# Kernel optimization log

Hardware: AMD Instinct MI355X
Metric: run time of the kernel (lower is better)

## Reference

```python
import jax, jax.numpy as jnp
import numpy as np

B, S, V, E, H = 128, 128, 8000, 512, 2048
GIVEN = 64


def setup_inputs() -> dict:
    key = jax.random.key(0)
    ks = jax.random.split(key, 13)
    def p(i, shape):
        return (jax.random.normal(ks[i], shape, jnp.float32) * 0.02)
    return {
        "x": jax.random.randint(ks[0], (B, S), 0, V, jnp.int32),
        "class_label": jax.random.randint(ks[1], (B,), 0, 2, jnp.int32),
        "given_num": GIVEN,
        "emb": p(2, (V, E)),
        "Wih0": p(3, (4 * H, E)), "Whh0": p(4, (4 * H, H)),
        "bih0": p(5, (4 * H,)), "bhh0": p(6, (4 * H,)),
        "Wih1": p(7, (4 * H, H)), "Whh1": p(8, (4 * H, H)),
        "bih1": p(9, (4 * H,)), "bhh1": p(10, (4 * H,)),
        "Wlin": p(11, (V, H)), "blin": p(12, (V,)),
    }


def _cell(xt, h, c, Wih, Whh, bih, bhh):
    # PyTorch LSTMCell math, gate order (i, f, g, o)
    g = xt @ Wih.T + h @ Whh.T + (bih + bhh)
    i, f, gg, o = jnp.split(g, 4, axis=-1)
    c = jax.nn.sigmoid(f) * c + jax.nn.sigmoid(i) * jnp.tanh(gg)
    h = jax.nn.sigmoid(o) * jnp.tanh(c)
    return h, c


def reference(x, class_label, given_num, emb, Wih0, Whh0, bih0, bhh0,
              Wih1, Whh1, bih1, bhh1, Wlin, blin):
    Bb, Ss = x.shape
    Hh = Whh0.shape[1]
    z = jnp.zeros((Bb, Hh), dtype=emb.dtype)
    init = (z, z, z, z)  # (h0, c0, h1, c1) for 2-layer LSTM

    def two_layer(carry, te):
        h0, c0, h1, c1 = carry
        h0, c0 = _cell(te, h0, c0, Wih0, Whh0, bih0, bhh0)
        h1, c1 = _cell(h0, h1, c1, Wih1, Whh1, bih1, bhh1)
        return (h0, c0, h1, c1)

    # Teacher-forced prefix: feed ground-truth tokens for i < given_num
    seq_e = emb[x[:, :given_num]]  # (B, given_num, E)
    def tf_step(carry, te):
        return two_layer(carry, te), None
    carry, _ = jax.lax.scan(tf_step, init, seq_e.swapaxes(0, 1))

    # Rollout: sample from softmax(logits) each step (multinomial == categorical)
    te0 = emb[x[:, given_num - 1]]  # (B, E)
    keys = jax.random.split(jax.random.key(1), Ss - given_num)

    def roll_step(carry, k):
        (h0, c0, h1, c1), te = carry
        h0, c0, h1, c1 = two_layer((h0, c0, h1, c1), te)
        logits = h1 @ Wlin.T + blin  # (B, V)
        nt = jax.random.categorical(k, logits)  # (B,)
        return ((h0, c0, h1, c1), emb[nt]), nt

    _, toks = jax.lax.scan(roll_step, (carry, te0), keys)  # (S-given, B)
    return jnp.concatenate([x[:, :given_num], toks.T.astype(x.dtype)], axis=1)
```

## Files before the change

### kernel.cpp

```cpp
#include <hip/hip_runtime.h>
#include <stdint.h>
#include <math.h>

#define B_     128
#define S_     128
#define V_     8000
#define E_     512
#define H_     2048
#define H4_    8192
#define GIVEN_ 64

typedef __bf16 bf16x8 __attribute__((ext_vector_type(8)));
typedef float  f32x16 __attribute__((ext_vector_type(16)));
typedef short  short8 __attribute__((ext_vector_type(8)));

__device__ __forceinline__ uint32_t rotl32(uint32_t v, int d) {
  return (v << d) | (v >> (32 - d));
}

__device__ __forceinline__ void threefry2x32(uint32_t k0, uint32_t k1,
                                             uint32_t x0, uint32_t x1,
                                             uint32_t& o0, uint32_t& o1) {
  uint32_t k2 = k0 ^ k1 ^ 0x1BD11BDAu;
  x0 += k0; x1 += k1;
#define TF_RND(R) { x0 += x1; x1 = rotl32(x1, (R)); x1 ^= x0; }
  TF_RND(13) TF_RND(15) TF_RND(26) TF_RND(6)
  x0 += k1; x1 += k2 + 1u;
  TF_RND(17) TF_RND(29) TF_RND(16) TF_RND(24)
  x0 += k2; x1 += k0 + 2u;
  TF_RND(13) TF_RND(15) TF_RND(26) TF_RND(6)
  x0 += k0; x1 += k1 + 3u;
  TF_RND(17) TF_RND(29) TF_RND(16) TF_RND(24)
  x0 += k1; x1 += k2 + 4u;
  TF_RND(13) TF_RND(15) TF_RND(26) TF_RND(6)
  x0 += k2; x1 += k0 + 5u;
#undef TF_RND
  o0 = x0; o1 = x1;
}

__global__ void keys_kernel(uint32_t* __restrict__ keys) {
  int t = threadIdx.x;
  uint32_t o0, o1;
  threefry2x32(0u, 1u, 0u, (uint32_t)t, o0, o1);
  keys[2 * t]     = o0;
  keys[2 * t + 1] = o1;
}

__global__ void copy_prefix(const int* __restrict__ x, int* __restrict__ out) {
  int idx = blockIdx.x * blockDim.x + threadIdx.x;
  int b = idx >> 6;
  int s = idx & 63;
  out[b * S_ + s] = x[b * S_ + s];
}

__device__ __forceinline__ void split2(float x, uint16_t& hi, uint16_t& lo) {
  uint32_t xb = __float_as_uint(x);
  hi = (uint16_t)(xb >> 16);
  float l = x - __uint_as_float(xb & 0xFFFF0000u);
  lo = (uint16_t)(__float_as_uint(l) >> 16);
}

__device__ __forceinline__ void splitpack(float4 a, float4 b,
                                          bf16x8& hi, bf16x8& lo) {
  float e[8] = {a.x, a.y, a.z, a.w, b.x, b.y, b.z, b.w};
  short8 h, l;
#pragma unroll
  for (int j = 0; j < 8; ++j) {
    uint16_t h16, l16;
    split2(e[j], h16, l16);
    h[j] = (short)h16;
    l[j] = (short)l16;
  }
  hi = __builtin_bit_cast(bf16x8, h);
  lo = __builtin_bit_cast(bf16x8, l);
}

__device__ __forceinline__ void unpack3(short8 hv, uint2 m, bf16x8& bh, bf16x8& bl) {
  short8 lv;
#pragma unroll
  for (int j = 0; j < 8; ++j) {
    uint32_t hbits = ((uint32_t)(uint16_t)hv[j]) << 16;
    uint32_t mbyte = ((j < 4 ? (m.x >> (8 * j)) : (m.y >> (8 * (j - 4)))) & 0xFFu);
    float xf = __uint_as_float(hbits | (mbyte << 8));
    float lf = xf - __uint_as_float(hbits);
    lv[j] = (short)(__float_as_uint(lf) >> 16);
  }
  bh = __builtin_bit_cast(bf16x8, hv);
  bl = __builtin_bit_cast(bf16x8, lv);
}

__global__ __launch_bounds__(256) void pack3(
    const float* __restrict__ W, uint16_t* __restrict__ PH,
    uint8_t* __restrict__ PM, int n8)
{
  int i = blockIdx.x * 256 + threadIdx.x;
  if (i >= n8) return;
  float4 a = ((const float4*)W)[2 * i];
  float4 b = ((const float4*)W)[2 * i + 1];
  float e[8] = {a.x, a.y, a.z, a.w, b.x, b.y, b.z, b.w};
  short8 h;
  uint32_t mlo = 0, mhi = 0;
#pragma unroll
  for (int j = 0; j < 8; ++j) {
    uint32_t xb = __float_as_uint(e[j]);
    h[j] = (short)(xb >> 16);
    uint32_t mb = (xb >> 8) & 0xFFu;
    if (j < 4) mlo |= mb << (8 * j);
    else       mhi |= mb << (8 * (j - 4));
  }
  *(short8*)&PH[(size_t)i * 8] = h;
  *(uint2*)&PM[(size_t)i * 8] = make_uint2(mlo, mhi);
}

#define MFMA_(a, b, c) __builtin_amdgcn_mfma_f32_32x32x16_bf16(a, b, c, 0, 0, 0)

template<bool GATHER>
__device__ __forceinline__ void run_phase_p(
    f32x16 (&acc)[4],
    const float* __restrict__ aF,
    const uint16_t* __restrict__ aHi, const uint16_t* __restrict__ aLo,
    const int* __restrict__ ridx, int rstride,
    const uint16_t* __restrict__ PH, const uint8_t* __restrict__ PM,
    int K, bool gateRe, int jb, int w, int lrow, int lgrp)
{
  const int nFS = K >> 7;
  const int wrow = gateRe ? ((lrow >> 3) * H_ + jb * 8 + (lrow & 7))
                          : (jb * 32 + lrow);
  const size_t bbase = (size_t)wrow * K + lgrp * 8;

  size_t aoff0, aoff1, aoff2, aoff3;
  if (GATHER) {
    aoff0 = (size_t)ridx[(size_t)(lrow)      * rstride] * E_ + lgrp * 8;
    aoff1 = (size_t)ridx[(size_t)(32 + lrow) * rstride] * E_ + lgrp * 8;
    aoff2 = (size_t)ridx[(size_t)(64 + lrow) * rstride] * E_ + lgrp * 8;
    aoff3 = (size_t)ridx[(size_t)(96 + lrow) * rstride] * E_ + lgrp * 8;
  } else {
    aoff0 = (size_t)lgrp * 256 + (size_t)lrow * 8;
    aoff1 = aoff0 + 512;
    aoff2 = aoff0 + 1024;
    aoff3 = aoff0 + 1536;
  }

  short8 bH[2]; uint2 bM[2];
  float4 gR0[2][2], gR1[2][2], gR2[2][2], gR3[2][2];
  bf16x8 sh0[2], sh1[2], sh2[2], sh3[2], sl0[2], sl1[2], sl2[2], sl3[2];

#define LOADFS(BUF, KS)                                                      \
  {                                                                          \
    const size_t bo = bbase + (size_t)(KS) * 16;                             \
    bH[BUF] = *(const short8*)(PH + bo);                                     \
    bM[BUF] = *(const uint2*)(PM + bo);                                      \
    if (GATHER) {                                                            \
      const float* a0 = aF + aoff0 + (size_t)(KS) * 16;                      \
      const float* a1 = aF + aoff1 + (size_t)(KS) * 16;                      \
      const float* a2 = aF + aoff2 + (size_t)(KS) * 16;                      \
      const float* a3 = aF + aoff3 + (size_t)(KS) * 16;                      \
      gR0[BUF][0] = ((const float4*)a0)[0]; gR0[BUF][1] = ((const float4*)a0)[1]; \
      gR1[BUF][0] = ((const float4*)a1)[0]; gR1[BUF][1] = ((const float4*)a1)[1]; \
      gR2[BUF][0] = ((const float4*)a2)[0]; gR2[BUF][1] = ((const float4*)a2)[1]; \
      gR3[BUF][0] = ((const float4*)a3)[0]; gR3[BUF][1] = ((const float4*)a3)[1]; \
    } else {                                                                 \
      size_t o0 = aoff0 + (size_t)(KS) * 2048;                               \
      size_t o1 = aoff1 + (size_t)(KS) * 2048;                               \
      size_t o2 = aoff2 + (size_t)(KS) * 2048;                               \
      size_t o3 = aoff3 + (size_t)(KS) * 2048;                               \
      sh0[BUF] = *(const bf16x8*)(aHi + o0); sl0[BUF] = *(const bf16x8*)(aLo + o0); \
      sh1[BUF] = *(const bf16x8*)(aHi + o1); sl1[BUF] = *(const bf16x8*)(aLo + o1); \
      sh2[BUF] = *(const bf16x8*)(aHi + o2); sl2[BUF] = *(const bf16x8*)(aLo + o2); \
      sh3[BUF] = *(const bf16x8*)(aHi + o3); sl3[BUF] = *(const bf16x8*)(aLo + o3); \
    }                                                                        \
  }

#define COMPFS(BUF)                                                          \
  {                                                                          \
    bf16x8 bh, bl;                                                           \
    unpack3(bH[BUF], bM[BUF], bh, bl);                                       \
    bf16x8 ah, al;                                                           \
    if (GATHER) splitpack(gR0[BUF][0], gR0[BUF][1], ah, al);                 \
    else { ah = sh0[BUF]; al = sl0[BUF]; }                                   \
    acc[0] = MFMA_(ah, bh, acc[0]);                                          \
    acc[0] = MFMA_(ah, bl, acc[0]);                                          \
    acc[0] = MFMA_(al, bh, acc[0]);                                          \
    if (GATHER) splitpack(gR1[BUF][0], gR1[BUF][1], ah, al);                 \
    else { ah = sh1[BUF]; al = sl1[BUF]; }                                   \
    acc[1] = MFMA_(ah, bh, acc[1]);                                          \
    acc[1] = MFMA_(ah, bl, acc[1]);                                          \
    acc[1] = MFMA_(al, bh, acc[1]);                                          \
    if (GATHER) splitpack(gR2[BUF][0], gR2[BUF][1], ah, al);                 \
    else { ah = sh2[BUF]; al = sl2[BUF]; }                                   \
    acc[2] = MFMA_(ah, bh, acc[2]);                                          \
    acc[2] = MFMA_(ah, bl, acc[2]);                                          \
    acc[2] = MFMA_(al, bh, acc[2]);                                          \
    if (GATHER) splitpack(gR3[BUF][0], gR3[BUF][1], ah, al);                 \
    else { ah = sh3[BUF]; al = sl3[BUF]; }                                   \
    acc[3] = MFMA_(ah, bh, acc[3]);                                          \
    acc[3] = MFMA_(ah, bl, acc[3]);                                          \
    acc[3] = MFMA_(al, bh, acc[3]);                                          \
  }

  int ks = w;
  LOADFS(0, ks); ks += 8;
  int rem = nFS;
  while (rem >= 2) {
    LOADFS(1, ks); ks += 8;
    COMPFS(0);
    if (rem > 2) { LOADFS(0, ks); ks += 8; }
    COMPFS(1);
    rem -= 2;
  }
#undef LOADFS
#undef COMPFS
}

template<int EPI, int GATHER1>
__global__ __launch_bounds__(512, 2) void gemm_ks_p(
    const float* __restrict__ a1F,
    const uint16_t* __restrict__ a1Hi, const uint16_t* __restrict__ a1Lo,
    const int* __restrict__ ridx, int rstride,
    const uint16_t* __restrict__ PH1, const uint8_t* __restrict__ PM1, int K1,
    const uint16_t* __restrict__ a2Hi, const uint16_t* __restrict__ a2Lo,
    const uint16_t* __restrict__ PH2, const uint8_t* __restrict__ PM2, int K2,
    const float* __restrict__ bih, const float* __restrict__ bhh,
    float* __restrict__ cState,
    uint16_t* __restrict__ hOutHi, uint16_t* __restrict__ hOutLo,
    const float* __restrict__ bias, float* __restrict__ Cout)
{
  __shared__ float red[4][128 * 32];

  const int jb   = blockIdx.x;
  const int tid  = threadIdx.x;
  const int w    = tid >> 6;
  const int lane = tid & 63;
  const int lrow = lane & 31;
  const int lgrp = lane >> 5;

  f32x16 acc[4];
#pragma unroll
  for (int mf = 0; mf < 4; ++mf)
#pragma unroll
    for (int r = 0; r < 16; ++r) acc[mf][r] = 0.0f;

  run_phase_p<GATHER1 != 0>(acc, a1F, a1Hi, a1Lo, ridx, rstride,
                            PH1, PM1, K1, EPI == 1, jb, w, lrow, lgrp);
  if (K2 > 0)
    run_phase_p<false>(acc, nullptr, a2Hi, a2Lo, nullptr, 0,
                       PH2, PM2, K2, EPI == 1, jb, w, lrow, lgrp);

  const int wl = w & 3;
  if (w < 4) {
#pragma unroll
    for (int mf = 0; mf < 4; ++mf)
#pragma unroll
      for (int r = 0; r < 16; ++r) {
        const int row = mf * 32 + (r & 3) + 8 * (r >> 2) + 4 * lgrp;
        red[wl][row * 32 + (lrow ^ (row & 31))] = acc[mf][r];
      }
  }
  __syncthreads();
  if (w >= 4) {
#pragma unroll
    for (int mf = 0; mf < 4; ++mf)
#pragma unroll
      for (int r = 0; r < 16; ++r) {
        const int row = mf * 32 + (r & 3) + 8 * (r >> 2) + 4 * lgrp;
        red[wl][row * 32 + (lrow ^ (row & 31))] += acc[mf][r];
      }
  }
  __syncthreads();

  if constexpr (EPI == 1) {
    const int b  = tid & 127;
    const int uh = (tid >> 7) * 2;
#pragma unroll
    for (int q = 0; q < 2; ++q) {
      const int u = uh + q;
      float gs[4];
#pragma unroll
      for (int g = 0; g < 4; ++g) {
        const int cs = (g * 8 + u) ^ (b & 31);
        gs[g] = ((red[0][b * 32 + cs] + red[1][b * 32 + cs])
                 + red[2][b * 32 + cs]) + red[3][b * 32 + cs];
      }
      const int n = jb * 8 + u;
      float gi = gs[0] + bih[n]          + bhh[n];
      float gf = gs[1] + bih[H_ + n]     + bhh[H_ + n];
      float gg = gs[2] + bih[2 * H_ + n] + bhh[2 * H_ + n];
      float go = gs[3] + bih[3 * H_ + n] + bhh[3 * H_ + n];
      float si = 1.f / (1.f + expf(-gi));
      float sf = 1.f / (1.f + expf(-gf));
      float so = 1.f / (1.f + expf(-go));
      const size_t ci = (size_t)b * H_ + n;
      float cv = sf * cState[ci] + si * tanhf(gg);
      cState[ci] = cv;
      float hv = so * tanhf(cv);
      uint16_t hh, hl;
      split2(hv, hh, hl);
      const size_t hoff = (size_t)((n >> 4) * 4 + (b >> 5)) * 512
                        + (size_t)((n >> 3) & 1) * 256
                        + (size_t)(b & 31) * 8 + (size_t)(n & 7);
      hOutHi[hoff] = hh;
      hOutLo[hoff] = hl;
    }
  } else {
    const int b  = tid & 127;
    const int ch = (tid >> 7) * 8;
#pragma unroll
    for (int q = 0; q < 8; ++q) {
      const int col = ch + q;
      const int cs  = col ^ (b & 31);
      float v = ((red[0][b * 32 + cs] + red[1][b * 32 + cs])
                 + red[2][b * 32 + cs]) + red[3][b * 32 + cs];
      Cout[(size_t)b * V_ + jb * 32 + col] = v + bias[jb * 32 + col];
    }
  }
}

template<bool GATHER>
__device__ __forceinline__ void run_phase_f(
    f32x16 (&acc)[4],
    const float* __restrict__ aF,
    const uint16_t* __restrict__ aHi, const uint16_t* __restrict__ aLo,
    const int* __restrict__ ridx, int rstride,
    const float* __restrict__ W, int K, bool gateRe,
    int jb, int w, int lrow, int lgrp)
{
  const int nFS = K >> 7;
  const int wrow = gateRe ? ((lrow >> 3) * H_ + jb * 8 + (lrow & 7))
                          : (jb * 32 + lrow);
  const float* bptr = W + (size_t)wrow * K + lgrp * 8;

  size_t aoff0, aoff1, aoff2, aoff3;
  if (GATHER) {
    aoff0 = (size_t)ridx[(size_t)(lrow)      * rstride] * E_ + lgrp * 8;
    aoff1 = (size_t)ridx[(size_t)(32 + lrow) * rstride] * E_ + lgrp * 8;
    aoff2 = (size_t)ridx[(size_t)(64 + lrow) * rstride] * E_ + lgrp * 8;
    aoff3 = (size_t)ridx[(size_t)(96 + lrow) * rstride] * E_ + lgrp * 8;
  } else {
    aoff0 = (size_t)lgrp * 256 + (size_t)lrow * 8;
    aoff1 = aoff0 + 512;
    aoff2 = aoff0 + 1024;
    aoff3 = aoff0 + 1536;
  }

  float4 bR0[2], bR1[2];
  float4 gR0[2][2], gR1[2][2], gR2[2][2], gR3[2][2];
  bf16x8 sh0[2], sh1[2], sh2[2], sh3[2], sl0[2], sl1[2], sl2[2], sl3[2];

#define LOADFS(BUF, KS)                                                      \
  {                                                                          \
    const float* bp = bptr + (size_t)(KS) * 16;                              \
    bR0[BUF] = ((const float4*)bp)[0];                                       \
    bR1[BUF] = ((const float4*)bp)[1];                                       \
    if (GATHER) {                                                            \
      const float* a0 = aF + aoff0 + (size_t)(KS) * 16;                      \
      const float* a1 = aF + aoff1 + (size_t)(KS) * 16;                      \
      const float* a2 = aF + aoff2 + (size_t)(KS) * 16;                      \
      const float* a3 = aF + aoff3 + (size_t)(KS) * 16;                      \
      gR0[BUF][0] = ((const float4*)a0)[0]; gR0[BUF][1] = ((const float4*)a0)[1]; \
      gR1[BUF][0] = ((const float4*)a1)[0]; gR1[BUF][1] = ((const float4*)a1)[1]; \
      gR2[BUF][0] = ((const float4*)a2)[0]; gR2[BUF][1] = ((const float4*)a2)[1]; \
      gR3[BUF][0] = ((const float4*)a3)[0]; gR3[BUF][1] = ((const float4*)a3)[1]; \
    } else {                                                                 \
      size_t o0 = aoff0 + (size_t)(KS) * 2048;                               \
      size_t o1 = aoff1 + (size_t)(KS) * 2048;                               \
      size_t o2 = aoff2 + (size_t)(KS) * 2048;                               \
      size_t o3 = aoff3 + (size_t)(KS) * 2048;                               \
      sh0[BUF] = *(const bf16x8*)(aHi + o0); sl0[BUF] = *(const bf16x8*)(aLo + o0); \
      sh1[BUF] = *(const bf16x8*)(aHi + o1); sl1[BUF] = *(const bf16x8*)(aLo + o1); \
      sh2[BUF] = *(const bf16x8*)(aHi + o2); sl2[BUF] = *(const bf16x8*)(aLo + o2); \
      sh3[BUF] = *(const bf16x8*)(aHi + o3); sl3[BUF] = *(const bf16x8*)(aLo + o3); \
    }                                                                        \
  }

#define COMPFS(BUF)                                                          \
  {                                                                          \
    bf16x8 bh, bl;                                                           \
    splitpack(bR0[BUF], bR1[BUF], bh, bl);                                   \
    bf16x8 ah, al;                                                           \
    if (GATHER) splitpack(gR0[BUF][0], gR0[BUF][1], ah, al);                 \
    else { ah = sh0[BUF]; al = sl0[BUF]; }                                   \
    acc[0] = MFMA_(ah, bh, acc[0]);                                          \
    acc[0] = MFMA_(ah, bl, acc[0]);                                          \
    acc[0] = MFMA_(al, bh, acc[0]);                                          \
    if (GATHER) splitpack(gR1[BUF][0], gR1[BUF][1], ah, al);                 \
    else { ah = sh1[BUF]; al = sl1[BUF]; }                                   \
    acc[1] = MFMA_(ah, bh, acc[1]);                                          \
    acc[1] = MFMA_(ah, bl, acc[1]);                                          \
    acc[1] = MFMA_(al, bh, acc[1]);                                          \
    if (GATHER) splitpack(gR2[BUF][0], gR2[BUF][1], ah, al);                 \
    else { ah = sh2[BUF]; al = sl2[BUF]; }                                   \
    acc[2] = MFMA_(ah, bh, acc[2]);                                          \
    acc[2] = MFMA_(ah, bl, acc[2]);                                          \
    acc[2] = MFMA_(al, bh, acc[2]);                                          \
    if (GATHER) splitpack(gR3[BUF][0], gR3[BUF][1], ah, al);                 \
    else { ah = sh3[BUF]; al = sl3[BUF]; }                                   \
    acc[3] = MFMA_(ah, bh, acc[3]);                                          \
    acc[3] = MFMA_(ah, bl, acc[3]);                                          \
    acc[3] = MFMA_(al, bh, acc[3]);                                          \
  }

  int ks = w;
  LOADFS(0, ks); ks += 8;
  int rem = nFS;
  while (rem >= 2) {
    LOADFS(1, ks); ks += 8;
    COMPFS(0);
    if (rem > 2) { LOADFS(0, ks); ks += 8; }
    COMPFS(1);
    rem -= 2;
  }
#undef LOADFS
#undef COMPFS
}

template<int EPI, int GATHER1>
__global__ __launch_bounds__(512, 2) void gemm_ks_f(
    const float* __restrict__ a1F,
    const uint16_t* __restrict__ a1Hi, const uint16_t* __restrict__ a1Lo,
    const int* __restrict__ ridx, int rstride,
    const float* __restrict__ W1, int K1,
    const uint16_t* __restrict__ a2Hi, const uint16_t* __restrict__ a2Lo,
    const float* __restrict__ W2, int K2,
    const float* __restrict__ bih, const float* __restrict__ bhh,
    float* __restrict__ cState,
    uint16_t* __restrict__ hOutHi, uint16_t* __restrict__ hOutLo,
    const float* __restrict__ bias, float* __restrict__ Cout)
{
  __shared__ float red[4][128 * 32];

  const int jb   = blockIdx.x;
  const int tid  = threadIdx.x;
  const int w    = tid >> 6;
  const int lane = tid & 63;
  const int lrow = lane & 31;
  const int lgrp = lane >> 5;

  f32x16 acc[4];
#pragma unroll
  for (int mf = 0; mf < 4; ++mf)
#pragma unroll
    for (int r = 0; r < 16; ++r) acc[mf][r] = 0.0f;

  run_phase_f<GATHER1 != 0>(acc, a1F, a1Hi, a1Lo, ridx, rstride,
                            W1, K1, EPI == 1, jb, w, lrow, lgrp);
  if (K2 > 0)
    run_phase_f<false>(acc, nullptr, a2Hi, a2Lo, nullptr, 0,
                       W2, K2, EPI == 1, jb, w, lrow, lgrp);

  const int wl = w & 3;
  if (w < 4) {
#pragma unroll
    for (int mf = 0; mf < 4; ++mf)
#pragma unroll
      for (int r = 0; r < 16; ++r) {
        const int row = mf * 32 + (r & 3) + 8 * (r >> 2) + 4 * lgrp;
        red[wl][row * 32 + (lrow ^ (row & 31))] = acc[mf][r];
      }
  }
  __syncthreads();
  if (w >= 4) {
#pragma unroll
    for (int mf = 0; mf < 4; ++mf)
#pragma unroll
      for (int r = 0; r < 16; ++r) {
        const int row = mf * 32 + (r & 3) + 8 * (r >> 2) + 4 * lgrp;
        red[wl][row * 32 + (lrow ^ (row & 31))] += acc[mf][r];
      }
  }
  __syncthreads();

  if constexpr (EPI == 1) {
    const int b  = tid & 127;
    const int uh = (tid >> 7) * 2;
#pragma unroll
    for (int q = 0; q < 2; ++q) {
      const int u = uh + q;
      float gs[4];
#pragma unroll
      for (int g = 0; g < 4; ++g) {
        const int cs = (g * 8 + u) ^ (b & 31);
        gs[g] = ((red[0][b * 32 + cs] + red[1][b * 32 + cs])
                 + red[2][b * 32 + cs]) + red[3][b * 32 + cs];
      }
      const int n = jb * 8 + u;
      float gi = gs[0] + bih[n]          + bhh[n];
      float gf = gs[1] + bih[H_ + n]     + bhh[H_ + n];
      float gg = gs[2] + bih[2 * H_ + n] + bhh[2 * H_ + n];
      float go = gs[3] + bih[3 * H_ + n] + bhh[3 * H_ + n];
      float si = 1.f / (1.f + expf(-gi));
      float sf = 1.f / (1.f + expf(-gf));
      float so = 1.f / (1.f + expf(-go));
      const size_t ci = (size_t)b * H_ + n;
      float cv = sf * cState[ci] + si * tanhf(gg);
      cState[ci] = cv;
      float hv = so * tanhf(cv);
      uint16_t hh, hl;
      split2(hv, hh, hl);
      const size_t hoff = (size_t)((n >> 4) * 4 + (b >> 5)) * 512
                        + (size_t)((n >> 3) & 1) * 256
                        + (size_t)(b & 31) * 8 + (size_t)(n & 7);
      hOutHi[hoff] = hh;
      hOutLo[hoff] = hl;
    }
  } else {
    const int b  = tid & 127;
    const int ch = (tid >> 7) * 8;
#pragma unroll
    for (int q = 0; q < 8; ++q) {
      const int col = ch + q;
      const int cs  = col ^ (b & 31);
      float v = ((red[0][b * 32 + cs] + red[1][b * 32 + cs])
                 + red[2][b * 32 + cs]) + red[3][b * 32 + cs];
      Cout[(size_t)b * V_ + jb * 32 + col] = v + bias[jb * 32 + col];
    }
  }
}

__global__ __launch_bounds__(256) void sample_kernel(
    const float* __restrict__ logits, const uint32_t* __restrict__ keys,
    int t, int* __restrict__ out, int col)
{
  const int b = blockIdx.x;
  const int tid = threadIdx.x;
  const uint32_t k0 = keys[2 * t];
  const uint32_t k1 = keys[2 * t + 1];
  const float* lrow = logits + (size_t)b * V_;

  float best = -3.4e38f;
  int bestIdx = 0;
  for (int v = tid; v < V_; v += 256) {
    uint32_t j = (uint32_t)(b * V_ + v);
    uint32_t o0, o1;
    threefry2x32(k0, k1, 0u, j, o0, o1);
    uint32_t bits = o0 ^ o1;
    float f = __uint_as_float((bits >> 9) | 0x3f800000u) - 1.0f;
    float u = fmaxf(1.17549435e-38f, f + 1.17549435e-38f);
    float t1 = (float)log((double)u);
    float t2 = -t1;
    float t3 = (float)log((double)t2);
    float val = (-t3) + lrow[v];
    if (val > best) { best = val; bestIdx = v; }
  }

  __shared__ float sv[256];
  __shared__ int   si[256];
  sv[tid] = best; si[tid] = bestIdx;
  __syncthreads();
  for (int s = 128; s > 0; s >>= 1) {
    if (tid < s) {
      float v2 = sv[tid + s]; int i2 = si[tid + s];
      if (v2 > sv[tid] || (v2 == sv[tid] && i2 < si[tid])) { sv[tid] = v2; si[tid] = i2; }
    }
    __syncthreads();
  }
  if (tid == 0) out[b * S_ + col] = si[0];
}

extern "C" void kernel_launch(void* const* d_in, const int* in_sizes, int n_in,
                              void* d_out, int out_size, void* d_ws, size_t ws_size,
                              hipStream_t stream) {
  const int*   x    = (const int*)  d_in[0];
  const float* emb  = (const float*)d_in[3];
  const float* Wih0 = (const float*)d_in[4];
  const float* Whh0 = (const float*)d_in[5];
  const float* bih0 = (const float*)d_in[6];
  const float* bhh0 = (const float*)d_in[7];
  const float* Wih1 = (const float*)d_in[8];
  const float* Whh1 = (const float*)d_in[9];
  const float* bih1 = (const float*)d_in[10];
  const float* bhh1 = (const float*)d_in[11];
  const float* Wlin = (const float*)d_in[12];
  const float* blin = (const float*)d_in[13];
  int* out = (int*)d_out;

  char* wp = (char*)d_ws;
  size_t o = 0;
  auto alloc = [&](size_t bytes) {
    void* p = wp + o; o += (bytes + 255) & ~(size_t)255; return p;
  };
  uint32_t* keys   = (uint32_t*)alloc(512);
  float*    logits = (float*)   alloc((size_t)B_ * V_ * 4);
  float*    c0     = (float*)   alloc((size_t)B_ * H_ * 4);
  float*    c1     = (float*)   alloc((size_t)B_ * H_ * 4);
  uint16_t* hS0hi[2]; uint16_t* hS0lo[2]; uint16_t* hS1hi[2]; uint16_t* hS1lo[2];
  for (int i = 0; i < 2; ++i) hS0hi[i] = (uint16_t*)alloc((size_t)B_ * H_ * 2);
  for (int i = 0; i < 2; ++i) hS0lo[i] = (uint16_t*)alloc((size_t)B_ * H_ * 2);
  for (int i = 0; i < 2; ++i) hS1hi[i] = (uint16_t*)alloc((size_t)B_ * H_ * 2);
  for (int i = 0; i < 2; ++i) hS1lo[i] = (uint16_t*)alloc((size_t)B_ * H_ * 2);
  size_t zeroBytes = (size_t)((char*)hS1lo[1] + (size_t)B_ * H_ * 2 - (char*)c0);

  const size_t nIh0 = (size_t)H4_ * E_;
  const size_t nHh  = (size_t)H4_ * H_;
  const size_t nLin = (size_t)V_ * H_;
  uint16_t* PHih0 = (uint16_t*)alloc(nIh0 * 2);
  uint8_t*  PMih0 = (uint8_t*) alloc(nIh0);
  uint16_t* PHhh0 = (uint16_t*)alloc(nHh * 2);
  uint8_t*  PMhh0 = (uint8_t*) alloc(nHh);
  uint16_t* PHih1 = (uint16_t*)alloc(nHh * 2);
  uint8_t*  PMih1 = (uint8_t*) alloc(nHh);
  uint16_t* PHhh1 = (uint16_t*)alloc(nHh * 2);
  uint8_t*  PMhh1 = (uint8_t*) alloc(nHh);
  uint16_t* PHlin = (uint16_t*)alloc(nLin * 2);
  uint8_t*  PMlin = (uint8_t*) alloc(nLin);
  const bool usePacked = (o <= ws_size);

  hipMemsetAsync(c0, 0, zeroBytes, stream);
  keys_kernel<<<1, 64, 0, stream>>>(keys);
  copy_prefix<<<(B_ * GIVEN_) / 256, 256, 0, stream>>>(x, out);

  if (usePacked) {
    pack3<<<(int)((nIh0 / 8 + 255) / 256), 256, 0, stream>>>(Wih0, PHih0, PMih0, (int)(nIh0 / 8));
    pack3<<<(int)((nHh / 8 + 255) / 256), 256, 0, stream>>>(Whh0, PHhh0, PMhh0, (int)(nHh / 8));
    pack3<<<(int)((nHh / 8 + 255) / 256), 256, 0, stream>>>(Wih1, PHih1, PMih1, (int)(nHh / 8));
    pack3<<<(int)((nHh / 8 + 255) / 256), 256, 0, stream>>>(Whh1, PHhh1, PMhh1, (int)(nHh / 8));
    pack3<<<(int)((nLin / 8 + 255) / 256), 256, 0, stream>>>(Wlin, PHlin, PMlin, (int)(nLin / 8));
  }

  int p = 0;
  auto lstm_step = [&](const int* ridx) {
    if (usePacked) {
      gemm_ks_p<1, 1><<<H_ / 8, 512, 0, stream>>>(
          emb, nullptr, nullptr, ridx, S_, PHih0, PMih0, E_,
          hS0hi[p], hS0lo[p], PHhh0, PMhh0, H_,
          bih0, bhh0, c0, hS0hi[p ^ 1], hS0lo[p ^ 1], nullptr, nullptr);
      gemm_ks_p<1, 0><<<H_ / 8, 512, 0, stream>>>(
          nullptr, hS0hi[p ^ 1], hS0lo[p ^ 1], nullptr, 0, PHih1, PMih1, H_,
          hS1hi[p], hS1lo[p], PHhh1, PMhh1, H_,
          bih1, bhh1, c1, hS1hi[p ^ 1], hS1lo[p ^ 1], nullptr, nullptr);
    } else {
      gemm_ks_f<1, 1><<<H_ / 8, 512, 0, stream>>>(
          emb, nullptr, nullptr, ridx, S_, Wih0, E_,
          hS0hi[p], hS0lo[p], Whh0, H_,
          bih0, bhh0, c0, hS0hi[p ^ 1], hS0lo[p ^ 1], nullptr, nullptr);
      gemm_ks_f<1, 0><<<H_ / 8, 512, 0, stream>>>(
          nullptr, hS0hi[p ^ 1], hS0lo[p ^ 1], nullptr, 0, Wih1, H_,
          hS1hi[p], hS1lo[p], Whh1, H_,
          bih1, bhh1, c1, hS1hi[p ^ 1], hS1lo[p ^ 1], nullptr, nullptr);
    }
    p ^= 1;
  };

  for (int t = 0; t < GIVEN_; ++t) {
    lstm_step(x + t);
  }

  for (int t = 0; t < S_ - GIVEN_; ++t) {
    const int* ridx = (t == 0) ? (x + (GIVEN_ - 1)) : (out + (GIVEN_ + t - 1));
    lstm_step(ridx);
    if (usePacked) {
      gemm_ks_p<0, 0><<<V_ / 32, 512, 0, stream>>>(
          nullptr, hS1hi[p], hS1lo[p], nullptr, 0, PHlin, PMlin, H_,
          nullptr, nullptr, nullptr, nullptr, 0,
          nullptr, nullptr, nullptr, nullptr, nullptr, blin, logits);
    } else {
      gemm_ks_f<0, 0><<<V_ / 32, 512, 0, stream>>>(
          nullptr, hS1hi[p], hS1lo[p], nullptr, 0, Wlin, H_,
          nullptr, nullptr, nullptr, 0,
          nullptr, nullptr, nullptr, nullptr, nullptr, blin, logits);
    }
    sample_kernel<<<B_, 256, 0, stream>>>(logits, keys, t, out, GIVEN_ + t);
  }
}
```

Before: 12.72 ms.

## Retile packed GEMM to 64x64 output tiles with 2D grid and deeper prefetch

The packed-weight GEMM kernel moves from a 128-batch by 32-column tile to a 64x64 tile, with a second grid dimension splitting the batch into two halves. Each wave now runs a 2x2 set of MFMA accumulators, so every loaded weight fragment is reused across two batch fragments and every activation fragment across two weight fragments. Weight loads are prefetched four k-steps ahead instead of one. The block count stays the same for the LSTM gates and drops from 250 to 250 (125x2) for the logits, but each block reads half the batch and twice the weight rows, which doubles total weight traffic across blocks while cutting per-block activation reuse pressure. The change also raises register use and depends on the new gate interleave and hidden-state store layout being correct.

```diff
diff --git a/kernel.cpp b/kernel.cpp
--- a/kernel.cpp
+++ b/kernel.cpp
@@ -115,18 +115,244 @@
 #define MFMA_(a, b, c) __builtin_amdgcn_mfma_f32_32x32x16_bf16(a, b, c, 0, 0, 0)
 
 template<bool GATHER>
-__device__ __forceinline__ void run_phase_p(
+__device__ __forceinline__ void run_phase64_p(
+    f32x16 (&acc)[2][2],
+    const float* __restrict__ aF,
+    const uint16_t* __restrict__ aHi, const uint16_t* __restrict__ aLo,
+    int tok0, int tok1,
+    const uint16_t* __restrict__ PH, const uint8_t* __restrict__ PM,
+    int K, bool gateRe, int jb, int mb, int w, int lrow, int lgrp)
+{
+  const int nFS = K >> 7;
+  const int c0 = lrow, c1 = 32 + lrow;
+  const int wrow0 = gateRe ? ((c0 >> 4) * H_ + jb * 16 + (c0 & 15)) : (jb * 64 + c0);
+  const int wrow1 = gateRe ? ((c1 >> 4) * H_ + jb * 16 + (c1 & 15)) : (jb * 64 + c1);
+  const size_t bb0 = (size_t)wrow0 * K + lgrp * 8;
+  const size_t bb1 = (size_t)wrow1 * K + lgrp * 8;
+
+  size_t aoff0, aoff1;
+  if (GATHER) {
+    aoff0 = (size_t)tok0 * E_ + lgrp * 8;
+    aoff1 = (size_t)tok1 * E_ + lgrp * 8;
+  } else {
+    aoff0 = (size_t)(mb * 2) * 512 + (size_t)lgrp * 256 + (size_t)lrow * 8;
+    aoff1 = aoff0 + 512;
+  }
+
+  short8 bH0[4], bH1[4]; uint2 bM0[4], bM1[4];
+  float4 gA0[2][2], gA1[2][2];
+  bf16x8 sh0[2], sh1[2], sl0[2], sl1[2];
+
+#define BLOAD(BUF, KS)                                                       \
+  {                                                                          \
+    const size_t o0 = bb0 + (size_t)(KS) * 16;                               \
+    const size_t o1 = bb1 + (size_t)(KS) * 16;                               \
+    bH0[BUF] = *(const short8*)(PH + o0);                                    \
+    bM0[BUF] = *(const uint2*)(PM + o0);                                     \
+    bH1[BUF] = *(const short8*)(PH + o1);                                    \
+    bM1[BUF] = *(const uint2*)(PM + o1);                                     \
+  }
+
+#define ALOAD(BUF, KS)                                                       \
+  {                                                                          \
+    if (GATHER) {                                                            \
+      const float* a0 = aF + aoff0 + (size_t)(KS) * 16;                      \
+      const float* a1 = aF + aoff1 + (size_t)(KS) * 16;                      \
+      gA0[BUF][0] = ((const float4*)a0)[0];                                  \
+      gA0[BUF][1] = ((const float4*)a0)[1];                                  \
+      gA1[BUF][0] = ((const float4*)a1)[0];                                  \
+      gA1[BUF][1] = ((const float4*)a1)[1];                                  \
+    } else {                                                                 \
+      size_t o0 = aoff0 + (size_t)(KS) * 2048;                               \
+      size_t o1 = aoff1 + (size_t)(KS) * 2048;                               \
+      sh0[BUF] = *(const bf16x8*)(aHi + o0);                                 \
+      sl0[BUF] = *(const bf16x8*)(aLo + o0);                                 \
+      sh1[BUF] = *(const bf16x8*)(aHi + o1);                                 \
+      sl1[BUF] = *(const bf16x8*)(aLo + o1);                                 \
+    }                                                                        \
+  }
+
+#define COMP(BB, AB)                                                         \
+  {                                                                          \
+    bf16x8 bh0, bl0, bh1, bl1;                                               \
+    unpack3(bH0[BB], bM0[BB], bh0, bl0);                                     \
+    unpack3(bH1[BB], bM1[BB], bh1, bl1);                                     \
+    bf16x8 ah0, al0, ah1, al1;                                               \
+    if (GATHER) {                                                            \
+      splitpack(gA0[AB][0], gA0[AB][1], ah0, al0);                           \
+      splitpack(gA1[AB][0], gA1[AB][1], ah1, al1);                           \
+    } else {                                                                 \
+      ah0 = sh0[AB]; al0 = sl0[AB];                                          \
+      ah1 = sh1[AB]; al1 = sl1[AB];                                          \
+    }                                                                        \
+    acc[0][0] = MFMA_(ah0, bh0, acc[0][0]);                                  \
+    acc[0][0] = MFMA_(ah0, bl0, acc[0][0]);                                  \
+    acc[0][0] = MFMA_(al0, bh0, acc[0][0]);                                  \
+    acc[0][1] = MFMA_(ah0, bh1, acc[0][1]);                                  \
+    acc[0][1] = MFMA_(ah0, bl1, acc[0][1]);                                  \
+    acc[0][1] = MFMA_(al0, bh1, acc[0][1]);                                  \
+    acc[1][0] = MFMA_(ah1, bh0, acc[1][0]);                                  \
+    acc[1][0] = MFMA_(ah1, bl0, acc[1][0]);                                  \
+    acc[1][0] = MFMA_(al1, bh0, acc[1][0]);                                  \
+    acc[1][1] = MFMA_(ah1, bh1, acc[1][1]);                                  \
+    acc[1][1] = MFMA_(ah1, bl1, acc[1][1]);                                  \
+    acc[1][1] = MFMA_(al1, bh1, acc[1][1]);                                  \
+  }
+
+  BLOAD(0, w); BLOAD(1, w + 8); BLOAD(2, w + 16); BLOAD(3, w + 24);
+  ALOAD(0, w); ALOAD(1, w + 8);
+  for (int it = 0; it < nFS; it += 4) {
+    const int kb = w + it * 8;
+    COMP(0, 0);
+    if (it + 4 < nFS) BLOAD(0, kb + 32);
+    if (it + 2 < nFS) ALOAD(0, kb + 16);
+    COMP(1, 1);
+    if (it + 5 < nFS) BLOAD(1, kb + 40);
+    if (it + 3 < nFS) ALOAD(1, kb + 24);
+    COMP(2, 0);
+    if (it + 6 < nFS) BLOAD(2, kb + 48);
+    if (it + 4 < nFS) ALOAD(0, kb + 32);
+    COMP(3, 1);
+    if (it + 7 < nFS) BLOAD(3, kb + 56);
+    if (it + 5 < nFS) ALOAD(1, kb + 40);
+  }
+#undef BLOAD
+#undef ALOAD
+#undef COMP
+}
+
+template<int EPI, int GATHER1>
+__global__ __launch_bounds__(512, 2) void gemm_ks_p(
+    const float* __restrict__ a1F,
+    const uint16_t* __restrict__ a1Hi, const uint16_t* __restrict__ a1Lo,
+    const int* __restrict__ ridx, int rstride,
+    const uint16_t* __restrict__ PH1, const uint8_t* __restrict__ PM1, int K1,
+    const uint16_t* __restrict__ a2Hi, const uint16_t* __restrict__ a2Lo,
+    const uint16_t* __restrict__ PH2, const uint8_t* __restrict__ PM2, int K2,
+    const float* __restrict__ bih, const float* __restrict__ bhh,
+    float* __restrict__ cState,
+    uint16_t* __restrict__ hOutHi, uint16_t* __restrict__ hOutLo,
+    const float* __restrict__ bias, float* __restrict__ Cout)
+{
+  __shared__ float red[4][64 * 64];
+
+  const int jb   = blockIdx.x;
+  const int mb   = blockIdx.y;
+  const int tid  = threadIdx.x;
+  const int w    = tid >> 6;
+  const int lane = tid & 63;
+  const int lrow = lane & 31;
+  const int lgrp = lane >> 5;
+
+  f32x16 acc[2][2];
+#pragma unroll
+  for (int i = 0; i < 2; ++i)
+#pragma unroll
+    for (int j = 0; j < 2; ++j)
+#pragma unroll
+      for (int r = 0; r < 16; ++r) acc[i][j][r] = 0.0f;
+
+  if (GATHER1) {
+    const int tok0 = ridx[(size_t)(mb * 64 + lrow) * rstride];
+    const int tok1 = ridx[(size_t)(mb * 64 + 32 + lrow) * rstride];
+    run_phase64_p<true>(acc, a1F, nullptr, nullptr, tok0, tok1,
+                        PH1, PM1, K1, EPI == 1, jb, mb, w, lrow, lgrp);
+  } else {
+    run_phase64_p<false>(acc, nullptr, a1Hi, a1Lo, 0, 0,
+                         PH1, PM1, K1, EPI == 1, jb, mb, w, lrow, lgrp);
+  }
+  if (K2 > 0)
+    run_phase64_p<false>(acc, nullptr, a2Hi, a2Lo, 0, 0,
+                         PH2, PM2, K2, EPI == 1, jb, mb, w, lrow, lgrp);
+
+  const int wl = w & 3;
+  if (w < 4) {
+#pragma unroll
+    for (int mf = 0; mf < 2; ++mf)
+#pragma unroll
+      for (int nf = 0; nf < 2; ++nf)
+#pragma unroll
+        for (int r = 0; r < 16; ++r) {
+          const int row = mf * 32 + (r & 3) + 8 * (r >> 2) + 4 * lgrp;
+          red[wl][row * 64 + nf * 32 + (lrow ^ (row & 31))] = acc[mf][nf][r];
+        }
+  }
+  __syncthreads();
+  if (w >= 4) {
+#pragma unroll
+    for (int mf = 0; mf < 2; ++mf)
+#pragma unroll
+      for (int nf = 0; nf < 2; ++nf)
+#pragma unroll
+        for (int r = 0; r < 16; ++r) {
+          const int row = mf * 32 + (r & 3) + 8 * (r >> 2) + 4 * lgrp;
+          red[wl][row * 64 + nf * 32 + (lrow ^ (row & 31))] += acc[mf][nf][r];
+        }
+  }
+  __syncthreads();
+
+  if constexpr (EPI == 1) {
+    const int b    = tid & 63;
+    const int brow = mb * 64 + b;
+    const int uh   = tid >> 6;
+#pragma unroll
+    for (int q = 0; q < 2; ++q) {
+      const int u = uh * 2 + q;
+      float gs[4];
+#pragma unroll
+      for (int g = 0; g < 4; ++g) {
+        const int cs = (g * 16 + u) ^ (b & 31);
+        gs[g] = ((red[0][b * 64 + cs] + red[1][b * 64 + cs])
+                 + red[2][b * 64 + cs]) + red[3][b * 64 + cs];
+      }
+      const int n = jb * 16 + u;
+      float gi = gs[0] + bih[n]          + bhh[n];
+      float gf = gs[1] + bih[H_ + n]     + bhh[H_ + n];
+      float gg = gs[2] + bih[2 * H_ + n] + bhh[2 * H_ + n];
+      float go = gs[3] + bih[3 * H_ + n] + bhh[3 * H_ + n];
+      float si = 1.f / (1.f + expf(-gi));
+      float sf = 1.f / (1.f + expf(-gf));
+      float so = 1.f / (1.f + expf(-go));
+      const size_t ci = (size_t)brow * H_ + n;
+      float cv = sf * cState[ci] + si * tanhf(gg);
+      cState[ci] = cv;
+      float hv = so * tanhf(cv);
+      uint16_t hh, hl;
+      split2(hv, hh, hl);
+      const size_t hoff = (size_t)((n >> 4) * 4 + (brow >> 5)) * 512
+                        + (size_t)((n >> 3) & 1) * 256
+                        + (size_t)(brow & 31) * 8 + (size_t)(n & 7);
+      hOutHi[hoff] = hh;
+      hOutLo[hoff] = hl;
+    }
+  } else {
+    const int b  = tid & 63;
+    const int bg = mb * 64 + b;
+    const int ch = (tid >> 6) * 8;
+#pragma unroll
+    for (int q = 0; q < 8; ++q) {
+      const int col = ch + q;
+      const int cs  = col ^ (b & 31);
+      float v = ((red[0][b * 64 + cs] + red[1][b * 64 + cs])
+                 + red[2][b * 64 + cs]) + red[3][b * 64 + cs];
+      Cout[(size_t)bg * V_ + jb * 64 + col] = v + bias[jb * 64 + col];
+    }
+  }
+}
+
+template<bool GATHER>
+__device__ __forceinline__ void run_phase_f(
     f32x16 (&acc)[4],
     const float* __restrict__ aF,
     const uint16_t* __restrict__ aHi, const uint16_t* __restrict__ aLo,
     const int* __restrict__ ridx, int rstride,
-    const uint16_t* __restrict__ PH, const uint8_t* __restrict__ PM,
-    int K, bool gateRe, int jb, int w, int lrow, int lgrp)
+    const float* __restrict__ W, int K, bool gateRe,
+    int jb, int w, int lrow, int lgrp)
 {
   const int nFS = K >> 7;
   const int wrow = gateRe ? ((lrow >> 3) * H_ + jb * 8 + (lrow & 7))
                           : (jb * 32 + lrow);
-  const size_t bbase = (size_t)wrow * K + lgrp * 8;
+  const float* bptr = W + (size_t)wrow * K + lgrp * 8;
 
   size_t aoff0, aoff1, aoff2, aoff3;
   if (GATHER) {
@@ -141,15 +367,15 @@
     aoff3 = aoff0 + 1536;
   }
 
-  short8 bH[2]; uint2 bM[2];
+  float4 bR0[2], bR1[2];
   float4 gR0[2][2], gR1[2][2], gR2[2][2], gR3[2][2];
   bf16x8 sh0[2], sh1[2], sh2[2], sh3[2], sl0[2], sl1[2], sl2[2], sl3[2];
 
 #define LOADFS(BUF, KS)                                                      \
   {                                                                          \
-    const size_t bo = bbase + (size_t)(KS) * 16;                             \
-    bH[BUF] = *(const short8*)(PH + bo);                                     \
-    bM[BUF] = *(const uint2*)(PM + bo);                                      \
+    const float* bp = bptr + (size_t)(KS) * 16;                              \
+    bR0[BUF] = ((const float4*)bp)[0];                                       \
+    bR1[BUF] = ((const float4*)bp)[1];                                       \
     if (GATHER) {                                                            \
       const float* a0 = aF + aoff0 + (size_t)(KS) * 16;                      \
       const float* a1 = aF + aoff1 + (size_t)(KS) * 16;                      \
@@ -174,7 +400,7 @@
 #define COMPFS(BUF)                                                          \
   {                                                                          \
     bf16x8 bh, bl;                                                           \
-    unpack3(bH[BUF], bM[BUF], bh, bl);                                       \
+    splitpack(bR0[BUF], bR1[BUF], bh, bl);                                   \
     bf16x8 ah, al;                                                           \
     if (GATHER) splitpack(gR0[BUF][0], gR0[BUF][1], ah, al);                 \
     else { ah = sh0[BUF]; al = sl0[BUF]; }                                   \
@@ -213,13 +439,13 @@
 }
 
 template<int EPI, int GATHER1>
-__global__ __launch_bounds__(512, 2) void gemm_ks_p(
+__global__ __launch_bounds__(512, 2) void gemm_ks_f(
     const float* __restrict__ a1F,
     const uint16_t* __restrict__ a1Hi, const uint16_t* __restrict__ a1Lo,
     const int* __restrict__ ridx, int rstride,
-    const uint16_t* __restrict__ PH1, const uint8_t* __restrict__ PM1, int K1,
+    const float* __restrict__ W1, int K1,
     const uint16_t* __restrict__ a2Hi, const uint16_t* __restrict__ a2Lo,
-    const uint16_t* __restrict__ PH2, const uint8_t* __restrict__ PM2, int K2,
+    const float* __restrict__ W2, int K2,
     const float* __restrict__ bih, const float* __restrict__ bhh,
     float* __restrict__ cState,
     uint16_t* __restrict__ hOutHi, uint16_t* __restrict__ hOutLo,
@@ -240,11 +466,11 @@
 #pragma unroll
     for (int r = 0; r < 16; ++r) acc[mf][r] = 0.0f;
 
-  run_phase_p<GATHER1 != 0>(acc, a1F, a1Hi, a1Lo, ridx, rstride,
-                            PH1, PM1, K1, EPI == 1, jb, w, lrow, lgrp);
+  run_phase_f<GATHER1 != 0>(acc, a1F, a1Hi, a1Lo, ridx, rstride,
+                            W1, K1, EPI == 1, jb, w, lrow, lgrp);
   if (K2 > 0)
-    run_phase_p<false>(acc, nullptr, a2Hi, a2Lo, nullptr, 0,
-                       PH2, PM2, K2, EPI == 1, jb, w, lrow, lgrp);
+    run_phase_f<false>(acc, nullptr, a2Hi, a2Lo, nullptr, 0,
+                       W2, K2, EPI == 1, jb, w, lrow, lgrp);
 
   const int wl = w & 3;
   if (w < 4) {
@@ -315,207 +541,6 @@
   }
 }
 
-template<bool GATHER>
-__device__ __forceinline__ void run_phase_f(
-    f32x16 (&acc)[4],
-    const float* __restrict__ aF,
-    const uint16_t* __restrict__ aHi, const uint16_t* __restrict__ aLo,
-    const int* __restrict__ ridx, int rstride,
-    const float* __restrict__ W, int K, bool gateRe,
-    int jb, int w, int lrow, int lgrp)
-{
-  const int nFS = K >> 7;
-  const int wrow = gateRe ? ((lrow >> 3) * H_ + jb * 8 + (lrow & 7))
-                          : (jb * 32 + lrow);
-  const float* bptr = W + (size_t)wrow * K + lgrp * 8;
-
-  size_t aoff0, aoff1, aoff2, aoff3;
-  if (GATHER) {
-    aoff0 = (size_t)ridx[(size_t)(lrow)      * rstride] * E_ + lgrp * 8;
-    aoff1 = (size_t)ridx[(size_t)(32 + lrow) * rstride] * E_ + lgrp * 8;
-    aoff2 = (size_t)ridx[(size_t)(64 + lrow) * rstride] * E_ + lgrp * 8;
-    aoff3 = (size_t)ridx[(size_t)(96 + lrow) * rstride] * E_ + lgrp * 8;
-  } else {
-    aoff0 = (size_t)lgrp * 256 + (size_t)lrow * 8;
-    aoff1 = aoff0 + 512;
-    aoff2 = aoff0 + 1024;
-    aoff3 = aoff0 + 1536;
-  }
-
-  float4 bR0[2], bR1[2];
-  float4 gR0[2][2], gR1[2][2], gR2[2][2], gR3[2][2];
-  bf16x8 sh0[2], sh1[2], sh2[2], sh3[2], sl0[2], sl1[2], sl2[2], sl3[2];
-
-#define LOADFS(BUF, KS)                                                      \
-  {                                                                          \
-    const float* bp = bptr + (size_t)(KS) * 16;                              \
-    bR0[BUF] = ((const float4*)bp)[0];                                       \
-    bR1[BUF] = ((const float4*)bp)[1];                                       \
-    if (GATHER) {                                                            \
-      const float* a0 = aF + aoff0 + (size_t)(KS) * 16;                      \
-      const float* a1 = aF + aoff1 + (size_t)(KS) * 16;                      \
-      const float* a2 = aF + aoff2 + (size_t)(KS) * 16;                      \
-      const float* a3 = aF + aoff3 + (size_t)(KS) * 16;                      \
-      gR0[BUF][0] = ((const float4*)a0)[0]; gR0[BUF][1] = ((const float4*)a0)[1]; \
-      gR1[BUF][0] = ((const float4*)a1)[0]; gR1[BUF][1] = ((const float4*)a1)[1]; \
-      gR2[BUF][0] = ((const float4*)a2)[0]; gR2[BUF][1] = ((const float4*)a2)[1]; \
-      gR3[BUF][0] = ((const float4*)a3)[0]; gR3[BUF][1] = ((const float4*)a3)[1]; \
-    } else {                                                                 \
-      size_t o0 = aoff0 + (size_t)(KS) * 2048;                               \
-      size_t o1 = aoff1 + (size_t)(KS) * 2048;                               \
-      size_t o2 = aoff2 + (size_t)(KS) * 2048;                               \
-      size_t o3 = aoff3 + (size_t)(KS) * 2048;                               \
-      sh0[BUF] = *(const bf16x8*)(aHi + o0); sl0[BUF] = *(const bf16x8*)(aLo + o0); \
-      sh1[BUF] = *(const bf16x8*)(aHi + o1); sl1[BUF] = *(const bf16x8*)(aLo + o1); \
-      sh2[BUF] = *(const bf16x8*)(aHi + o2); sl2[BUF] = *(const bf16x8*)(aLo + o2); \
-      sh3[BUF] = *(const bf16x8*)(aHi + o3); sl3[BUF] = *(const bf16x8*)(aLo + o3); \
-    }                                                                        \
-  }
-
-#define COMPFS(BUF)                                                          \
-  {                                                                          \
-    bf16x8 bh, bl;                                                           \
-    splitpack(bR0[BUF], bR1[BUF], bh, bl);                                   \
-    bf16x8 ah, al;                                                           \
-    if (GATHER) splitpack(gR0[BUF][0], gR0[BUF][1], ah, al);                 \
-    else { ah = sh0[BUF]; al = sl0[BUF]; }                                   \
-    acc[0] = MFMA_(ah, bh, acc[0]);                                          \
-    acc[0] = MFMA_(ah, bl, acc[0]);                                          \
-    acc[0] = MFMA_(al, bh, acc[0]);                                          \
-    if (GATHER) splitpack(gR1[BUF][0], gR1[BUF][1], ah, al);                 \
-    else { ah = sh1[BUF]; al = sl1[BUF]; }                                   \
-    acc[1] = MFMA_(ah, bh, acc[1]);                                          \
-    acc[1] = MFMA_(ah, bl, acc[1]);                                          \
-    acc[1] = MFMA_(al, bh, acc[1]);                                          \
-    if (GATHER) splitpack(gR2[BUF][0], gR2[BUF][1], ah, al);                 \
-    else { ah = sh2[BUF]; al = sl2[BUF]; }                                   \
-    acc[2] = MFMA_(ah, bh, acc[2]);                                          \
-    acc[2] = MFMA_(ah, bl, acc[2]);                                          \
-    acc[2] = MFMA_(al, bh, acc[2]);                                          \
-    if (GATHER) splitpack(gR3[BUF][0], gR3[BUF][1], ah, al);                 \
-    else { ah = sh3[BUF]; al = sl3[BUF]; }                                   \
-    acc[3] = MFMA_(ah, bh, acc[3]);                                          \
-    acc[3] = MFMA_(ah, bl, acc[3]);                                          \
-    acc[3] = MFMA_(al, bh, acc[3]);                                          \
-  }
-
-  int ks = w;
-  LOADFS(0, ks); ks += 8;
-  int rem = nFS;
-  while (rem >= 2) {
-    LOADFS(1, ks); ks += 8;
-    COMPFS(0);
-    if (rem > 2) { LOADFS(0, ks); ks += 8; }
-    COMPFS(1);
-    rem -= 2;
-  }
-#undef LOADFS
-#undef COMPFS
-}
-
-template<int EPI, int GATHER1>
-__global__ __launch_bounds__(512, 2) void gemm_ks_f(
-    const float* __restrict__ a1F,
-    const uint16_t* __restrict__ a1Hi, const uint16_t* __restrict__ a1Lo,
-    const int* __restrict__ ridx, int rstride,
-    const float* __restrict__ W1, int K1,
-    const uint16_t* __restrict__ a2Hi, const uint16_t* __restrict__ a2Lo,
-    const float* __restrict__ W2, int K2,
-    const float* __restrict__ bih, const float* __restrict__ bhh,
-    float* __restrict__ cState,
-    uint16_t* __restrict__ hOutHi, uint16_t* __restrict__ hOutLo,
-    const float* __restrict__ bias, float* __restrict__ Cout)
-{
-  __shared__ float red[4][128 * 32];
-
-  const int jb   = blockIdx.x;
-  const int tid  = threadIdx.x;
-  const int w    = tid >> 6;
-  const int lane = tid & 63;
-  const int lrow = lane & 31;
-  const int lgrp = lane >> 5;
-
-  f32x16 acc[4];
-#pragma unroll
-  for (int mf = 0; mf < 4; ++mf)
-#pragma unroll
-    for (int r = 0; r < 16; ++r) acc[mf][r] = 0.0f;
-
-  run_phase_f<GATHER1 != 0>(acc, a1F, a1Hi, a1Lo, ridx, rstride,
-                            W1, K1, EPI == 1, jb, w, lrow, lgrp);
-  if (K2 > 0)
-    run_phase_f<false>(acc, nullptr, a2Hi, a2Lo, nullptr, 0,
-                       W2, K2, EPI == 1, jb, w, lrow, lgrp);
-
-  const int wl = w & 3;
-  if (w < 4) {
-#pragma unroll
-    for (int mf = 0; mf < 4; ++mf)
-#pragma unroll
-      for (int r = 0; r < 16; ++r) {
-        const int row = mf * 32 + (r & 3) + 8 * (r >> 2) + 4 * lgrp;
-        red[wl][row * 32 + (lrow ^ (row & 31))] = acc[mf][r];
-      }
-  }
-  __syncthreads();
-  if (w >= 4) {
-#pragma unroll
-    for (int mf = 0; mf < 4; ++mf)
-#pragma unroll
-      for (int r = 0; r < 16; ++r) {
-        const int row = mf * 32 + (r & 3) + 8 * (r >> 2) + 4 * lgrp;
-        red[wl][row * 32 + (lrow ^ (row & 31))] += acc[mf][r];
-      }
-  }
-  __syncthreads();
-
-  if constexpr (EPI == 1) {
-    const int b  = tid & 127;
-    const int uh = (tid >> 7) * 2;
-#pragma unroll
-    for (int q = 0; q < 2; ++q) {
-      const int u = uh + q;
-      float gs[4];
-#pragma unroll
-      for (int g = 0; g < 4; ++g) {
-        const int cs = (g * 8 + u) ^ (b & 31);
-        gs[g] = ((red[0][b * 32 + cs] + red[1][b * 32 + cs])
-                 + red[2][b * 32 + cs]) + red[3][b * 32 + cs];
-      }
-      const int n = jb * 8 + u;
-      float gi = gs[0] + bih[n]          + bhh[n];
-      float gf = gs[1] + bih[H_ + n]     + bhh[H_ + n];
-      float gg = gs[2] + bih[2 * H_ + n] + bhh[2 * H_ + n];
-      float go = gs[3] + bih[3 * H_ + n] + bhh[3 * H_ + n];
-      float si = 1.f / (1.f + expf(-gi));
-      float sf = 1.f / (1.f + expf(-gf));
-      float so = 1.f / (1.f + expf(-go));
-      const size_t ci = (size_t)b * H_ + n;
-      float cv = sf * cState[ci] + si * tanhf(gg);
-      cState[ci] = cv;
-      float hv = so * tanhf(cv);
-      uint16_t hh, hl;
-      split2(hv, hh, hl);
-      const size_t hoff = (size_t)((n >> 4) * 4 + (b >> 5)) * 512
-                        + (size_t)((n >> 3) & 1) * 256
-                        + (size_t)(b & 31) * 8 + (size_t)(n & 7);
-      hOutHi[hoff] = hh;
-      hOutLo[hoff] = hl;
-    }
-  } else {
-    const int b  = tid & 127;
-    const int ch = (tid >> 7) * 8;
-#pragma unroll
-    for (int q = 0; q < 8; ++q) {
-      const int col = ch + q;
-      const int cs  = col ^ (b & 31);
-      float v = ((red[0][b * 32 + cs] + red[1][b * 32 + cs])
-                 + red[2][b * 32 + cs]) + red[3][b * 32 + cs];
-      Cout[(size_t)b * V_ + jb * 32 + col] = v + bias[jb * 32 + col];
-    }
-  }
-}
-
 __global__ __launch_bounds__(256) void sample_kernel(
     const float* __restrict__ logits, const uint32_t* __restrict__ keys,
     int t, int* __restrict__ out, int col)
@@ -616,14 +641,17 @@
     pack3<<<(int)((nLin / 8 + 255) / 256), 256, 0, stream>>>(Wlin, PHlin, PMlin, (int)(nLin / 8));
   }
 
+  dim3 gridLSTM64(H4_ / 64, 2);
+  dim3 gridLogit64(V_ / 64, 2);
+
   int p = 0;
   auto lstm_step = [&](const int* ridx) {
     if (usePacked) {
-      gemm_ks_p<1, 1><<<H_ / 8, 512, 0, stream>>>(
+      gemm_ks_p<1, 1><<<gridLSTM64, 512, 0, stream>>>(
           emb, nullptr, nullptr, ridx, S_, PHih0, PMih0, E_,
           hS0hi[p], hS0lo[p], PHhh0, PMhh0, H_,
           bih0, bhh0, c0, hS0hi[p ^ 1], hS0lo[p ^ 1], nullptr, nullptr);
-      gemm_ks_p<1, 0><<<H_ / 8, 512, 0, stream>>>(
+      gemm_ks_p<1, 0><<<gridLSTM64, 512, 0, stream>>>(
           nullptr, hS0hi[p ^ 1], hS0lo[p ^ 1], nullptr, 0, PHih1, PMih1, H_,
           hS1hi[p], hS1lo[p], PHhh1, PMhh1, H_,
           bih1, bhh1, c1, hS1hi[p ^ 1], hS1lo[p ^ 1], nullptr, nullptr);
@@ -648,7 +676,7 @@
     const int* ridx = (t == 0) ? (x + (GIVEN_ - 1)) : (out + (GIVEN_ + t - 1));
     lstm_step(ridx);
     if (usePacked) {
-      gemm_ks_p<0, 0><<<V_ / 32, 512, 0, stream>>>(
+      gemm_ks_p<0, 0><<<gridLogit64, 512, 0, stream>>>(
           nullptr, hS1hi[p], hS1lo[p], nullptr, 0, PHlin, PMlin, H_,
           nullptr, nullptr, nullptr, nullptr, 0,
           nullptr, nullptr, nullptr, nullptr, nullptr, blin, logits);
```

After: 14.04 ms. 10.4% more time.

## Pre-permute packed weights into per-block panel layout for contiguous fragment loads

Applied to the files above, without the earlier changes.

The weight packing kernel now writes hi/mid bytes in a tiled panel order that matches the MFMA B-fragment access pattern, with each (row block, k-slice) stored as 64 contiguous lanes. The GEMM loads then read fully contiguous 16-byte and 8-byte chunks per wavefront instead of strided rows 2K apart, which should improve coalescing and cache-line use when streaming weights. The gate-reordering row mapping moves out of the hot kernel into the one-time pack. The cost is a pack kernel with many more small 64-thread blocks and strided reads.

```diff
diff --git a/kernel.cpp b/kernel.cpp
--- a/kernel.cpp
+++ b/kernel.cpp
@@ -89,14 +89,19 @@
   bl = __builtin_bit_cast(bf16x8, lv);
 }
 
-__global__ __launch_bounds__(256) void pack3(
+__global__ void pack3_panel(
     const float* __restrict__ W, uint16_t* __restrict__ PH,
-    uint8_t* __restrict__ PM, int n8)
+    uint8_t* __restrict__ PM, int K, int nks, int gateRe)
 {
-  int i = blockIdx.x * 256 + threadIdx.x;
-  if (i >= n8) return;
-  float4 a = ((const float4*)W)[2 * i];
-  float4 b = ((const float4*)W)[2 * i + 1];
+  const int bid = blockIdx.x;
+  const int jb = bid / nks, ks = bid - jb * nks;
+  const int t = threadIdx.x;
+  const int lrow = t & 31, lgrp = t >> 5;
+  const int wrow = gateRe ? ((lrow >> 3) * H_ + jb * 8 + (lrow & 7))
+                          : (jb * 32 + lrow);
+  const float* src = W + (size_t)wrow * K + ks * 16 + lgrp * 8;
+  float4 a = ((const float4*)src)[0];
+  float4 b = ((const float4*)src)[1];
   float e[8] = {a.x, a.y, a.z, a.w, b.x, b.y, b.z, b.w};
   short8 h;
   uint32_t mlo = 0, mhi = 0;
@@ -108,8 +113,9 @@
     if (j < 4) mlo |= mb << (8 * j);
     else       mhi |= mb << (8 * (j - 4));
   }
-  *(short8*)&PH[(size_t)i * 8] = h;
-  *(uint2*)&PM[(size_t)i * 8] = make_uint2(mlo, mhi);
+  const size_t bi = ((size_t)bid * 64 + t) * 8;
+  *(short8*)&PH[bi] = h;
+  *(uint2*)&PM[bi] = make_uint2(mlo, mhi);
 }
 
 #define MFMA_(a, b, c) __builtin_amdgcn_mfma_f32_32x32x16_bf16(a, b, c, 0, 0, 0)
@@ -121,12 +127,10 @@
     const uint16_t* __restrict__ aHi, const uint16_t* __restrict__ aLo,
     const int* __restrict__ ridx, int rstride,
     const uint16_t* __restrict__ PH, const uint8_t* __restrict__ PM,
-    int K, bool gateRe, int jb, int w, int lrow, int lgrp)
+    int K, int jb, int w, int lane, int lrow, int lgrp)
 {
   const int nFS = K >> 7;
-  const int wrow = gateRe ? ((lrow >> 3) * H_ + jb * 8 + (lrow & 7))
-                          : (jb * 32 + lrow);
-  const size_t bbase = (size_t)wrow * K + lgrp * 8;
+  const size_t bbase = (size_t)jb * (K >> 4);
 
   size_t aoff0, aoff1, aoff2, aoff3;
   if (GATHER) {
@@ -147,9 +151,9 @@
 
 #define LOADFS(BUF, KS)                                                      \
   {                                                                          \
-    const size_t bo = bbase + (size_t)(KS) * 16;                             \
-    bH[BUF] = *(const short8*)(PH + bo);                                     \
-    bM[BUF] = *(const uint2*)(PM + bo);                                      \
+    const size_t bi = ((bbase + (size_t)(KS)) * 64 + (size_t)lane) * 8;      \
+    bH[BUF] = *(const short8*)(PH + bi);                                     \
+    bM[BUF] = *(const uint2*)(PM + bi);                                      \
     if (GATHER) {                                                            \
       const float* a0 = aF + aoff0 + (size_t)(KS) * 16;                      \
       const float* a1 = aF + aoff1 + (size_t)(KS) * 16;                      \
@@ -241,10 +245,10 @@
     for (int r = 0; r < 16; ++r) acc[mf][r] = 0.0f;
 
   run_phase_p<GATHER1 != 0>(acc, a1F, a1Hi, a1Lo, ridx, rstride,
-                            PH1, PM1, K1, EPI == 1, jb, w, lrow, lgrp);
+                            PH1, PM1, K1, jb, w, lane, lrow, lgrp);
   if (K2 > 0)
     run_phase_p<false>(acc, nullptr, a2Hi, a2Lo, nullptr, 0,
-                       PH2, PM2, K2, EPI == 1, jb, w, lrow, lgrp);
+                       PH2, PM2, K2, jb, w, lane, lrow, lgrp);
 
   const int wl = w & 3;
   if (w < 4) {
@@ -609,11 +613,11 @@
   copy_prefix<<<(B_ * GIVEN_) / 256, 256, 0, stream>>>(x, out);
 
   if (usePacked) {
-    pack3<<<(int)((nIh0 / 8 + 255) / 256), 256, 0, stream>>>(Wih0, PHih0, PMih0, (int)(nIh0 / 8));
-    pack3<<<(int)((nHh / 8 + 255) / 256), 256, 0, stream>>>(Whh0, PHhh0, PMhh0, (int)(nHh / 8));
-    pack3<<<(int)((nHh / 8 + 255) / 256), 256, 0, stream>>>(Wih1, PHih1, PMih1, (int)(nHh / 8));
-    pack3<<<(int)((nHh / 8 + 255) / 256), 256, 0, stream>>>(Whh1, PHhh1, PMhh1, (int)(nHh / 8));
-    pack3<<<(int)((nLin / 8 + 255) / 256), 256, 0, stream>>>(Wlin, PHlin, PMlin, (int)(nLin / 8));
+    pack3_panel<<<256 * 32,  64, 0, stream>>>(Wih0, PHih0, PMih0, E_, 32, 1);
+    pack3_panel<<<256 * 128, 64, 0, stream>>>(Whh0, PHhh0, PMhh0, H_, 128, 1);
+    pack3_panel<<<256 * 128, 64, 0, stream>>>(Wih1, PHih1, PMih1, H_, 128, 1);
+    pack3_panel<<<256 * 128, 64, 0, stream>>>(Whh1, PHhh1, PMhh1, H_, 128, 1);
+    pack3_panel<<<250 * 128, 64, 0, stream>>>(Wlin, PHlin, PMlin, H_, 128, 0);
   }
 
   int p = 0;
```

New measurement: 10.97 ms. 1.16x faster.
